# Performance work log

Hardware: AMD Instinct MI355X
Metric: run time of the kernel (lower is better)

Reference implementation:

```python
import jax, jax.numpy as jnp
import numpy as np

DIM = 64
NUM_HEADS = 8
HEAD_DIM = DIM // NUM_HEADS
INF = 1e9
EPS = 1e-10
S, R = 2048, 512  # n_seq (MSA rows), n_res


def setup_inputs() -> dict:
    key = jax.random.key(0)
    ks = jax.random.split(key, 8)
    m = jax.random.normal(ks[0], (S, R, DIM), dtype=jnp.float32)
    attn_mask = jnp.ones((S, R), dtype=jnp.float32)
    # weights stored as [in, out] (torch Linear applies x @ W.T; equivalent math)
    Wq = jax.random.normal(ks[1], (DIM, NUM_HEADS * HEAD_DIM), dtype=jnp.float32) * (DIM ** -0.5)
    Wk = jax.random.normal(ks[2], (DIM, HEAD_DIM), dtype=jnp.float32) * (DIM ** -0.5)
    Wv = jax.random.normal(ks[3], (DIM, HEAD_DIM), dtype=jnp.float32) * (DIM ** -0.5)
    Wg = jax.random.normal(ks[4], (DIM, NUM_HEADS * HEAD_DIM), dtype=jnp.float32) * (DIM ** -0.5)
    bg = jnp.ones((NUM_HEADS * HEAD_DIM,), dtype=jnp.float32)  # gating init: bias=1
    Wo = jax.random.normal(ks[5], (NUM_HEADS * HEAD_DIM, DIM), dtype=jnp.float32) * (DIM ** -0.5)
    bo = jnp.zeros((DIM,), dtype=jnp.float32)
    return {"m": m, "attn_mask": attn_mask, "Wq": Wq, "Wk": Wk, "Wv": Wv,
            "Wg": Wg, "bg": bg, "Wo": Wo, "bo": bo}


def reference(m, attn_mask, Wq, Wk, Wv, Wg, bg, Wo, bo):
    # masked mean-pool over residue axis -> per-row query  [S, dim]
    q = jnp.sum(m * attn_mask[..., None], axis=-2) / (jnp.sum(attn_mask, axis=-1)[..., None] + EPS)
    q = (q @ Wq).reshape(S, NUM_HEADS, HEAD_DIM) * (HEAD_DIM ** -0.5)  # [S, H, hd]
    k = m @ Wk  # [S, R, hd] (single shared K/V head)
    v = m @ Wv  # [S, R, hd]
    a = jnp.einsum('shc,src->shr', q, k)  # [S, H, R]
    a = a + (INF * (attn_mask - 1.0))[:, None, :]
    a = jax.nn.softmax(a, axis=-1)
    o = jnp.einsum('shr,src->shc', a, v)  # [S, H, hd]
    g = jax.nn.sigmoid(m @ Wg + bg).reshape(S, R, NUM_HEADS, HEAD_DIM)  # [S, R, H, hd]
    o = o[:, None, :, :] * g  # broadcast pooled output across residues
    o = o.reshape(S, R, NUM_HEADS * HEAD_DIM)
    return o @ Wo + bo  # [S, R, dim]
```

## Files before the change

kernel.cpp:

```cpp
#include <hip/hip_runtime.h>
#include <hip/hip_bf16.h>
#include <math.h>

#define NS 2048
#define NR 512
#define ND 64
#define NH 8
#define NSLOT 18

typedef __attribute__((ext_vector_type(4))) float f4;
typedef __attribute__((ext_vector_type(4))) unsigned u4;
typedef __attribute__((ext_vector_type(2))) unsigned u2;
typedef __attribute__((ext_vector_type(8))) short s8;

__device__ __forceinline__ short f2bf(float f) {
  unsigned u = __builtin_bit_cast(unsigned, f);
  u += 0x7fffu + ((u >> 16) & 1u);
  return (short)(u >> 16);
}
__device__ __forceinline__ unsigned cvtpk(float lo, float hi) {
  unsigned r;
  asm("v_cvt_pk_bf16_f32 %0, %1, %2" : "=v"(r) : "v"(lo), "v"(hi));
  return r;
}
__device__ __forceinline__ float bflo(unsigned u) { return __builtin_bit_cast(float, u << 16); }
__device__ __forceinline__ float bfhi(unsigned u) { return __builtin_bit_cast(float, u & 0xffff0000u); }

__device__ __forceinline__ int swz(int r, int c) {
  return ((r << 7) + (c << 1)) ^ ((r & 7) << 4);
}
__device__ __forceinline__ int kvaddr(int r, int c) {
  return ((r << 5) + (c << 1)) ^ ((r & 4) << 2);
}

__global__ void prep_kernel(const float* __restrict__ Wk, const float* __restrict__ Wv,
                            const float* __restrict__ Wg, const float* __restrict__ Wo,
                            short* __restrict__ ws) {
  for (int i = threadIdx.x; i < NSLOT * 64; i += blockDim.x) {
    const int slot = i >> 6, lane = i & 63;
    const int col = lane & 15, kq = (lane >> 4) * 8;
    s8 f;
    if (slot < 2) {
      #pragma unroll
      for (int jj = 0; jj < 8; ++jj) {
        const int k = slot * 32 + kq + jj;
        f[jj] = f2bf(col < 8 ? Wk[k * 8 + col] : Wv[k * 8 + col - 8]);
      }
    } else if (slot < 10) {
      const int idx = slot - 2, ks = idx >> 2, nt = idx & 3;
      #pragma unroll
      for (int jj = 0; jj < 8; ++jj) {
        const int k = ks * 32 + kq + jj;
        f[jj] = f2bf(Wg[k * 64 + 4 * col + nt]);
      }
    } else {
      const int idx = slot - 10, ks = idx >> 2, nt = idx & 3;
      #pragma unroll
      for (int jj = 0; jj < 8; ++jj) {
        const int k = ks * 32 + kq + jj;
        f[jj] = f2bf(Wo[k * 64 + 4 * col + nt]);
      }
    }
    *reinterpret_cast<s8*>(ws + (size_t)i * 8) = f;
  }
}

__global__ __launch_bounds__(512, 6)
void ga_kernel(const float* __restrict__ gm, const float* __restrict__ gmask,
               const float* __restrict__ Wq, const float* __restrict__ bgp,
               const float* __restrict__ bop, const short* __restrict__ ws,
               float* __restrict__ gout)
{
  __shared__ short fragB[NSLOT * 64 * 8];
  __shared__ union {
    unsigned short kv[NR][16];
    short tmp[8][16 * ND];
  } ukv;
  __shared__ float maskb[NR];
  __shared__ float red[8][ND];
  __shared__ float ofl[ND];
  __shared__ float bgo[2][ND];

  const int t    = threadIdx.x;
  const int lane = t & 63;
  const int wv   = t >> 6;
  const int s    = blockIdx.x;

  const int arow = lane & 15;
  const int g    = lane >> 4;
  const int kq   = g * 8;

  const float* mrow = gm + (size_t)s * NR * ND;

  for (int i = t; i < NR; i += 512) maskb[i] = gmask[(size_t)s * NR + i];
  for (int i = t; i < NSLOT * 64; i += 512)
    *reinterpret_cast<s8*>(&fragB[i * 8]) =
        *reinterpret_cast<const s8*>(ws + (size_t)i * 8);
  if (t < 64)            bgo[0][t]      = bgp[t];
  else if (t < 128)      bgo[1][t - 64] = bop[t - 64];
  __syncthreads();

  f4 pA0 = {0,0,0,0}, pA1 = {0,0,0,0}, pB0 = {0,0,0,0}, pB1 = {0,0,0,0};
  #pragma unroll
  for (int mt = 0; mt < 4; ++mt) {
    const int row = wv * 64 + mt * 16 + arow;
    const float mk = maskb[row];
    const float* p = mrow + row * ND + kq;
    const f4 a0 = *reinterpret_cast<const f4*>(p);
    const f4 a1 = *reinterpret_cast<const f4*>(p + 4);
    const f4 b0 = *reinterpret_cast<const f4*>(p + 32);
    const f4 b1 = *reinterpret_cast<const f4*>(p + 36);
    pA0 += a0 * mk; pA1 += a1 * mk; pB0 += b0 * mk; pB1 += b1 * mk;
    u4 ua, ub;
    ua[0] = cvtpk(a0.x, a0.y); ua[1] = cvtpk(a0.z, a0.w);
    ua[2] = cvtpk(a1.x, a1.y); ua[3] = cvtpk(a1.z, a1.w);
    ub[0] = cvtpk(b0.x, b0.y); ub[1] = cvtpk(b0.z, b0.w);
    ub[2] = cvtpk(b1.x, b1.y); ub[3] = cvtpk(b1.z, b1.w);
    const s8 mA = __builtin_bit_cast(s8, ua);
    const s8 mB = __builtin_bit_cast(s8, ub);
    const s8 kf0 = *reinterpret_cast<const s8*>(&fragB[(0 * 64 + lane) * 8]);
    const s8 kf1 = *reinterpret_cast<const s8*>(&fragB[(1 * 64 + lane) * 8]);
    f4 acc = {0,0,0,0};
    acc = __builtin_amdgcn_mfma_f32_16x16x32_bf16(mA, kf0, acc, 0, 0, 0);
    acc = __builtin_amdgcn_mfma_f32_16x16x32_bf16(mB, kf1, acc, 0, 0, 0);
    const int r0 = wv * 64 + mt * 16;
    #pragma unroll
    for (int q = 0; q < 4; ++q)
      *reinterpret_cast<unsigned short*>(
          reinterpret_cast<char*>(ukv.kv) + kvaddr(r0 + g * 4 + q, arow)) =
          (unsigned short)f2bf(acc[q]);
  }
  #pragma unroll
  for (int off = 8; off >= 1; off >>= 1) {
    pA0.x += __shfl_xor(pA0.x, off); pA0.y += __shfl_xor(pA0.y, off);
    pA0.z += __shfl_xor(pA0.z, off); pA0.w += __shfl_xor(pA0.w, off);
    pA1.x += __shfl_xor(pA1.x, off); pA1.y += __shfl_xor(pA1.y, off);
    pA1.z += __shfl_xor(pA1.z, off); pA1.w += __shfl_xor(pA1.w, off);
    pB0.x += __shfl_xor(pB0.x, off); pB0.y += __shfl_xor(pB0.y, off);
    pB0.z += __shfl_xor(pB0.z, off); pB0.w += __shfl_xor(pB0.w, off);
    pB1.x += __shfl_xor(pB1.x, off); pB1.y += __shfl_xor(pB1.y, off);
    pB1.z += __shfl_xor(pB1.z, off); pB1.w += __shfl_xor(pB1.w, off);
  }
  if (arow == 0) {
    *reinterpret_cast<f4*>(&red[wv][kq])          = pA0;
    *reinterpret_cast<f4*>(&red[wv][kq + 4])      = pA1;
    *reinterpret_cast<f4*>(&red[wv][32 + kq])     = pB0;
    *reinterpret_cast<f4*>(&red[wv][32 + kq + 4]) = pB1;
  }
  __syncthreads();

  f4 pf0, pf1, pf2, pf3;
  {
    const float* p = mrow + (wv * 64 + arow) * ND + kq;
    pf0 = *reinterpret_cast<const f4*>(p);
    pf1 = *reinterpret_cast<const f4*>(p + 4);
    pf2 = *reinterpret_cast<const f4*>(p + 32);
    pf3 = *reinterpret_cast<const f4*>(p + 36);
  }

  float q0, q1, q2, q3, q4, q5, q6, q7;
  {
    float qv_l = 0.f;
    #pragma unroll
    for (int p = 0; p < 8; ++p) qv_l += red[p][lane];
    float dn = 0.f;
    #pragma unroll
    for (int i = 0; i < 8; ++i) dn += maskb[lane + 64 * i];
    #pragma unroll
    for (int off = 32; off; off >>= 1) dn += __shfl_xor(dn, off);
    const f4 w0 = *reinterpret_cast<const f4*>(Wq + lane * 64 + wv * 8);
    const f4 w1 = *reinterpret_cast<const f4*>(Wq + lane * 64 + wv * 8 + 4);
    float a0 = qv_l * w0.x, a1 = qv_l * w0.y, a2 = qv_l * w0.z, a3 = qv_l * w0.w;
    float a4 = qv_l * w1.x, a5 = qv_l * w1.y, a6 = qv_l * w1.z, a7 = qv_l * w1.w;
    #pragma unroll
    for (int off = 32; off; off >>= 1) {
      a0 += __shfl_xor(a0, off); a1 += __shfl_xor(a1, off);
      a2 += __shfl_xor(a2, off); a3 += __shfl_xor(a3, off);
      a4 += __shfl_xor(a4, off); a5 += __shfl_xor(a5, off);
      a6 += __shfl_xor(a6, off); a7 += __shfl_xor(a7, off);
    }
    const float qs = 0.35355339059327373f / (dn + 1e-10f);
    q0 = a0 * qs; q1 = a1 * qs; q2 = a2 * qs; q3 = a3 * qs;
    q4 = a4 * qs; q5 = a5 * qs; q6 = a6 * qs; q7 = a7 * qs;
  }

  {
    float lg[8];
    float mx = -3.4e38f;
    #pragma unroll
    for (int i = 0; i < 8; ++i) {
      const int r = lane + 64 * i;
      const u4 kk = *reinterpret_cast<const u4*>(
          reinterpret_cast<const char*>(ukv.kv) + ((r << 5) ^ ((r & 4) << 2)));
      float acc = q0 * bflo(kk[0]) + q1 * bfhi(kk[0])
                + q2 * bflo(kk[1]) + q3 * bfhi(kk[1])
                + q4 * bflo(kk[2]) + q5 * bfhi(kk[2])
                + q6 * bflo(kk[3]) + q7 * bfhi(kk[3]);
      lg[i] = acc + 1e9f * (maskb[r] - 1.0f);
      mx = fmaxf(mx, lg[i]);
    }
    #pragma unroll
    for (int off = 32; off; off >>= 1) mx = fmaxf(mx, __shfl_xor(mx, off));
    float sum = 0.f;
    #pragma unroll
    for (int i = 0; i < 8; ++i) { lg[i] = __expf(lg[i] - mx); sum += lg[i]; }
    #pragma unroll
    for (int off = 32; off; off >>= 1) sum += __shfl_xor(sum, off);
    const float inv = 1.0f / sum;
    float po[8] = {0,0,0,0,0,0,0,0};
    #pragma unroll
    for (int i = 0; i < 8; ++i) {
      const int r = lane + 64 * i;
      const float a = lg[i] * inv;
      const u4 vvv = *reinterpret_cast<const u4*>(
          reinterpret_cast<const char*>(ukv.kv) + (((r << 5) + 16) ^ ((r & 4) << 2)));
      po[0] += a * bflo(vvv[0]); po[1] += a * bfhi(vvv[0]);
      po[2] += a * bflo(vvv[1]); po[3] += a * bfhi(vvv[1]);
      po[4] += a * bflo(vvv[2]); po[5] += a * bfhi(vvv[2]);
      po[6] += a * bflo(vvv[3]); po[7] += a * bfhi(vvv[3]);
    }
    #pragma unroll
    for (int off = 32; off; off >>= 1) {
      #pragma unroll
      for (int c = 0; c < 8; ++c) po[c] += __shfl_xor(po[c], off);
    }
    #pragma unroll
    for (int c = 0; c < 8; ++c) if (lane == c) ofl[wv * 8 + c] = po[c];
  }
  __syncthreads();

  short* tmpw = &ukv.tmp[wv][0];
  float* orow_base = gout + (size_t)s * NR * ND;
  const f4 zf = {0,0,0,0};

  #pragma unroll
  for (int mt = 0; mt < 4; ++mt) {
    const int r0 = wv * 64 + mt * 16;
    f4 a0, a1, b0, b1;
    if (mt == 0) { a0 = pf0; a1 = pf1; b0 = pf2; b1 = pf3; }
    else {
      const float* p = mrow + (r0 + arow) * ND + kq;
      a0 = *reinterpret_cast<const f4*>(p);
      a1 = *reinterpret_cast<const f4*>(p + 4);
      b0 = *reinterpret_cast<const f4*>(p + 32);
      b1 = *reinterpret_cast<const f4*>(p + 36);
    }
    u4 ua, ub;
    ua[0] = cvtpk(a0.x, a0.y); ua[1] = cvtpk(a0.z, a0.w);
    ua[2] = cvtpk(a1.x, a1.y); ua[3] = cvtpk(a1.z, a1.w);
    ub[0] = cvtpk(b0.x, b0.y); ub[1] = cvtpk(b0.z, b0.w);
    ub[2] = cvtpk(b1.x, b1.y); ub[3] = cvtpk(b1.z, b1.w);
    const s8 mA = __builtin_bit_cast(s8, ua);
    const s8 mB = __builtin_bit_cast(s8, ub);

    f4 accG[4] = {zf, zf, zf, zf};
    #pragma unroll
    for (int nt = 0; nt < 4; ++nt) {
      const s8 wg0 = *reinterpret_cast<const s8*>(&fragB[((2 + nt) * 64 + lane) * 8]);
      const s8 wg1 = *reinterpret_cast<const s8*>(&fragB[((6 + nt) * 64 + lane) * 8]);
      accG[nt] = __builtin_amdgcn_mfma_f32_16x16x32_bf16(mA, wg0, accG[nt], 0, 0, 0);
      accG[nt] = __builtin_amdgcn_mfma_f32_16x16x32_bf16(mB, wg1, accG[nt], 0, 0, 0);
    }

    const f4 ofv = *reinterpret_cast<const f4*>(&ofl[4 * arow]);
    const f4 bgv = *reinterpret_cast<const f4*>(&bgo[0][4 * arow]);
    #pragma unroll
    for (int q = 0; q < 4; ++q) {
      float v[4];
      #pragma unroll
      for (int nt = 0; nt < 4; ++nt)
        v[nt] = ofv[nt] / (1.0f + __expf(-(accG[nt][q] + bgv[nt])));
      u2 w;
      w[0] = cvtpk(v[0], v[1]);
      w[1] = cvtpk(v[2], v[3]);
      *reinterpret_cast<u2*>(reinterpret_cast<char*>(tmpw) + swz(g * 4 + q, 4 * arow)) = w;
    }
    asm volatile("s_waitcnt lgkmcnt(0)" ::: "memory");
    __builtin_amdgcn_sched_barrier(0);

    f4 accO[4] = {zf, zf, zf, zf};
    #pragma unroll
    for (int ks = 0; ks < 2; ++ks) {
      const s8 aF = *reinterpret_cast<const s8*>(
          reinterpret_cast<const char*>(tmpw) + swz(arow, ks * 32 + kq));
      #pragma unroll
      for (int nt = 0; nt < 4; ++nt) {
        const s8 woF = *reinterpret_cast<const s8*>(&fragB[((10 + ks * 4 + nt) * 64 + lane) * 8]);
        accO[nt] = __builtin_amdgcn_mfma_f32_16x16x32_bf16(aF, woF, accO[nt], 0, 0, 0);
      }
    }
    const f4 bov = *reinterpret_cast<const f4*>(&bgo[1][4 * arow]);
    #pragma unroll
    for (int q = 0; q < 4; ++q) {
      f4 ov;
      ov.x = accO[0][q] + bov.x;
      ov.y = accO[1][q] + bov.y;
      ov.z = accO[2][q] + bov.z;
      ov.w = accO[3][q] + bov.w;
      *reinterpret_cast<f4*>(orow_base + (r0 + g * 4 + q) * ND + 4 * arow) = ov;
    }
  }
}

extern "C" void kernel_launch(void* const* d_in, const int* in_sizes, int n_in,
                              void* d_out, int out_size, void* d_ws, size_t ws_size,
                              hipStream_t stream) {
  const float* m    = (const float*)d_in[0];
  const float* mask = (const float*)d_in[1];
  const float* Wq   = (const float*)d_in[2];
  const float* Wk   = (const float*)d_in[3];
  const float* Wv   = (const float*)d_in[4];
  const float* Wg   = (const float*)d_in[5];
  const float* bg   = (const float*)d_in[6];
  const float* Wo   = (const float*)d_in[7];
  const float* bo   = (const float*)d_in[8];
  float* out = (float*)d_out;
  short* ws  = (short*)d_ws;

  prep_kernel<<<dim3(1), dim3(512), 0, stream>>>(Wk, Wv, Wg, Wo, ws);
  ga_kernel<<<dim3(NS), dim3(512), 0, stream>>>(m, mask, Wq, bg, bo, ws, out);
}
```

Measured before the change: 152.8 us.

## Halve block size to 256 threads and read weight fragments from global

Each block now uses 4 waves instead of 8. Each wave handles 128 rows and two heads of the attention, and the occupancy hint rises to 8 blocks. The shared-memory copy of the bf16 weight fragments is removed, and the fragments are loaded straight from the workspace in global memory, where they should stay in cache. This shrinks LDS use and per-block sync cost, but each wave does more sequential work. It also trades LDS reads for global/L2 reads inside the inner MFMA loops, and the prefetch of the first m tile is dropped.

```diff
diff --git a/kernel.cpp b/kernel.cpp
--- a/kernel.cpp
+++ b/kernel.cpp
@@ -65,19 +65,18 @@
   }
 }
 
-__global__ __launch_bounds__(512, 6)
+__global__ __launch_bounds__(256, 8)
 void ga_kernel(const float* __restrict__ gm, const float* __restrict__ gmask,
                const float* __restrict__ Wq, const float* __restrict__ bgp,
                const float* __restrict__ bop, const short* __restrict__ ws,
                float* __restrict__ gout)
 {
-  __shared__ short fragB[NSLOT * 64 * 8];
   __shared__ union {
     unsigned short kv[NR][16];
-    short tmp[8][16 * ND];
+    short tmp[4][16 * ND];
   } ukv;
   __shared__ float maskb[NR];
-  __shared__ float red[8][ND];
+  __shared__ float red[4][ND];
   __shared__ float ofl[ND];
   __shared__ float bgo[2][ND];
 
@@ -92,18 +91,17 @@
 
   const float* mrow = gm + (size_t)s * NR * ND;
 
-  for (int i = t; i < NR; i += 512) maskb[i] = gmask[(size_t)s * NR + i];
-  for (int i = t; i < NSLOT * 64; i += 512)
-    *reinterpret_cast<s8*>(&fragB[i * 8]) =
-        *reinterpret_cast<const s8*>(ws + (size_t)i * 8);
+  for (int i = t; i < NR; i += 256) maskb[i] = gmask[(size_t)s * NR + i];
   if (t < 64)            bgo[0][t]      = bgp[t];
   else if (t < 128)      bgo[1][t - 64] = bop[t - 64];
+  const s8 kf0 = *reinterpret_cast<const s8*>(ws + (size_t)(0 * 64 + lane) * 8);
+  const s8 kf1 = *reinterpret_cast<const s8*>(ws + (size_t)(1 * 64 + lane) * 8);
   __syncthreads();
 
   f4 pA0 = {0,0,0,0}, pA1 = {0,0,0,0}, pB0 = {0,0,0,0}, pB1 = {0,0,0,0};
   #pragma unroll
-  for (int mt = 0; mt < 4; ++mt) {
-    const int row = wv * 64 + mt * 16 + arow;
+  for (int mt = 0; mt < 8; ++mt) {
+    const int row = wv * 128 + mt * 16 + arow;
     const float mk = maskb[row];
     const float* p = mrow + row * ND + kq;
     const f4 a0 = *reinterpret_cast<const f4*>(p);
@@ -118,12 +116,10 @@
     ub[2] = cvtpk(b1.x, b1.y); ub[3] = cvtpk(b1.z, b1.w);
     const s8 mA = __builtin_bit_cast(s8, ua);
     const s8 mB = __builtin_bit_cast(s8, ub);
-    const s8 kf0 = *reinterpret_cast<const s8*>(&fragB[(0 * 64 + lane) * 8]);
-    const s8 kf1 = *reinterpret_cast<const s8*>(&fragB[(1 * 64 + lane) * 8]);
     f4 acc = {0,0,0,0};
     acc = __builtin_amdgcn_mfma_f32_16x16x32_bf16(mA, kf0, acc, 0, 0, 0);
     acc = __builtin_amdgcn_mfma_f32_16x16x32_bf16(mB, kf1, acc, 0, 0, 0);
-    const int r0 = wv * 64 + mt * 16;
+    const int r0 = wv * 128 + mt * 16;
     #pragma unroll
     for (int q = 0; q < 4; ++q)
       *reinterpret_cast<unsigned short*>(
@@ -149,42 +145,36 @@
   }
   __syncthreads();
 
-  f4 pf0, pf1, pf2, pf3;
+  float qv_l, qs;
   {
-    const float* p = mrow + (wv * 64 + arow) * ND + kq;
-    pf0 = *reinterpret_cast<const f4*>(p);
-    pf1 = *reinterpret_cast<const f4*>(p + 4);
-    pf2 = *reinterpret_cast<const f4*>(p + 32);
-    pf3 = *reinterpret_cast<const f4*>(p + 36);
-  }
-
-  float q0, q1, q2, q3, q4, q5, q6, q7;
-  {
-    float qv_l = 0.f;
-    #pragma unroll
-    for (int p = 0; p < 8; ++p) qv_l += red[p][lane];
+    qv_l = red[0][lane] + red[1][lane] + red[2][lane] + red[3][lane];
     float dn = 0.f;
     #pragma unroll
     for (int i = 0; i < 8; ++i) dn += maskb[lane + 64 * i];
     #pragma unroll
     for (int off = 32; off; off >>= 1) dn += __shfl_xor(dn, off);
-    const f4 w0 = *reinterpret_cast<const f4*>(Wq + lane * 64 + wv * 8);
-    const f4 w1 = *reinterpret_cast<const f4*>(Wq + lane * 64 + wv * 8 + 4);
-    float a0 = qv_l * w0.x, a1 = qv_l * w0.y, a2 = qv_l * w0.z, a3 = qv_l * w0.w;
-    float a4 = qv_l * w1.x, a5 = qv_l * w1.y, a6 = qv_l * w1.z, a7 = qv_l * w1.w;
-    #pragma unroll
-    for (int off = 32; off; off >>= 1) {
-      a0 += __shfl_xor(a0, off); a1 += __shfl_xor(a1, off);
-      a2 += __shfl_xor(a2, off); a3 += __shfl_xor(a3, off);
-      a4 += __shfl_xor(a4, off); a5 += __shfl_xor(a5, off);
-      a6 += __shfl_xor(a6, off); a7 += __shfl_xor(a7, off);
-    }
-    const float qs = 0.35355339059327373f / (dn + 1e-10f);
-    q0 = a0 * qs; q1 = a1 * qs; q2 = a2 * qs; q3 = a3 * qs;
-    q4 = a4 * qs; q5 = a5 * qs; q6 = a6 * qs; q7 = a7 * qs;
-  }
-
-  {
+    qs = 0.35355339059327373f / (dn + 1e-10f);
+  }
+
+  #pragma unroll
+  for (int h2 = 0; h2 < 2; ++h2) {
+    const int h = wv * 2 + h2;
+    float q0, q1, q2, q3, q4, q5, q6, q7;
+    {
+      const f4 w0 = *reinterpret_cast<const f4*>(Wq + lane * 64 + h * 8);
+      const f4 w1 = *reinterpret_cast<const f4*>(Wq + lane * 64 + h * 8 + 4);
+      float a0 = qv_l * w0.x, a1 = qv_l * w0.y, a2 = qv_l * w0.z, a3 = qv_l * w0.w;
+      float a4 = qv_l * w1.x, a5 = qv_l * w1.y, a6 = qv_l * w1.z, a7 = qv_l * w1.w;
+      #pragma unroll
+      for (int off = 32; off; off >>= 1) {
+        a0 += __shfl_xor(a0, off); a1 += __shfl_xor(a1, off);
+        a2 += __shfl_xor(a2, off); a3 += __shfl_xor(a3, off);
+        a4 += __shfl_xor(a4, off); a5 += __shfl_xor(a5, off);
+        a6 += __shfl_xor(a6, off); a7 += __shfl_xor(a7, off);
+      }
+      q0 = a0 * qs; q1 = a1 * qs; q2 = a2 * qs; q3 = a3 * qs;
+      q4 = a4 * qs; q5 = a5 * qs; q6 = a6 * qs; q7 = a7 * qs;
+    }
     float lg[8];
     float mx = -3.4e38f;
     #pragma unroll
@@ -225,26 +215,25 @@
       for (int c = 0; c < 8; ++c) po[c] += __shfl_xor(po[c], off);
     }
     #pragma unroll
-    for (int c = 0; c < 8; ++c) if (lane == c) ofl[wv * 8 + c] = po[c];
+    for (int c = 0; c < 8; ++c) if (lane == c) ofl[h * 8 + c] = po[c];
   }
   __syncthreads();
 
   short* tmpw = &ukv.tmp[wv][0];
   float* orow_base = gout + (size_t)s * NR * ND;
   const f4 zf = {0,0,0,0};
+  const f4 ofv = *reinterpret_cast<const f4*>(&ofl[4 * arow]);
+  const f4 bgv = *reinterpret_cast<const f4*>(&bgo[0][4 * arow]);
+  const f4 bov = *reinterpret_cast<const f4*>(&bgo[1][4 * arow]);
 
   #pragma unroll
-  for (int mt = 0; mt < 4; ++mt) {
-    const int r0 = wv * 64 + mt * 16;
-    f4 a0, a1, b0, b1;
-    if (mt == 0) { a0 = pf0; a1 = pf1; b0 = pf2; b1 = pf3; }
-    else {
-      const float* p = mrow + (r0 + arow) * ND + kq;
-      a0 = *reinterpret_cast<const f4*>(p);
-      a1 = *reinterpret_cast<const f4*>(p + 4);
-      b0 = *reinterpret_cast<const f4*>(p + 32);
-      b1 = *reinterpret_cast<const f4*>(p + 36);
-    }
+  for (int mt = 0; mt < 8; ++mt) {
+    const int r0 = wv * 128 + mt * 16;
+    const float* p = mrow + (r0 + arow) * ND + kq;
+    const f4 a0 = *reinterpret_cast<const f4*>(p);
+    const f4 a1 = *reinterpret_cast<const f4*>(p + 4);
+    const f4 b0 = *reinterpret_cast<const f4*>(p + 32);
+    const f4 b1 = *reinterpret_cast<const f4*>(p + 36);
     u4 ua, ub;
     ua[0] = cvtpk(a0.x, a0.y); ua[1] = cvtpk(a0.z, a0.w);
     ua[2] = cvtpk(a1.x, a1.y); ua[3] = cvtpk(a1.z, a1.w);
@@ -256,14 +245,12 @@
     f4 accG[4] = {zf, zf, zf, zf};
     #pragma unroll
     for (int nt = 0; nt < 4; ++nt) {
-      const s8 wg0 = *reinterpret_cast<const s8*>(&fragB[((2 + nt) * 64 + lane) * 8]);
-      const s8 wg1 = *reinterpret_cast<const s8*>(&fragB[((6 + nt) * 64 + lane) * 8]);
+      const s8 wg0 = *reinterpret_cast<const s8*>(ws + (size_t)((2 + nt) * 64 + lane) * 8);
+      const s8 wg1 = *reinterpret_cast<const s8*>(ws + (size_t)((6 + nt) * 64 + lane) * 8);
       accG[nt] = __builtin_amdgcn_mfma_f32_16x16x32_bf16(mA, wg0, accG[nt], 0, 0, 0);
       accG[nt] = __builtin_amdgcn_mfma_f32_16x16x32_bf16(mB, wg1, accG[nt], 0, 0, 0);
     }
 
-    const f4 ofv = *reinterpret_cast<const f4*>(&ofl[4 * arow]);
-    const f4 bgv = *reinterpret_cast<const f4*>(&bgo[0][4 * arow]);
     #pragma unroll
     for (int q = 0; q < 4; ++q) {
       float v[4];
@@ -285,11 +272,10 @@
           reinterpret_cast<const char*>(tmpw) + swz(arow, ks * 32 + kq));
       #pragma unroll
       for (int nt = 0; nt < 4; ++nt) {
-        const s8 woF = *reinterpret_cast<const s8*>(&fragB[((10 + ks * 4 + nt) * 64 + lane) * 8]);
+        const s8 woF = *reinterpret_cast<const s8*>(ws + (size_t)((10 + ks * 4 + nt) * 64 + lane) * 8);
         accO[nt] = __builtin_amdgcn_mfma_f32_16x16x32_bf16(aF, woF, accO[nt], 0, 0, 0);
       }
     }
-    const f4 bov = *reinterpret_cast<const f4*>(&bgo[1][4 * arow]);
     #pragma unroll
     for (int q = 0; q < 4; ++q) {
       f4 ov;
@@ -317,6 +303,6 @@
   float* out = (float*)d_out;
   short* ws  = (short*)d_ws;
 
-  prep_kernel<<<dim3(1), dim3(512), 0, stream>>>(Wk, Wv, Wg, Wo, ws);
-  ga_kernel<<<dim3(NS), dim3(512), 0, stream>>>(m, mask, Wq, bg, bo, ws, out);
-}
+  prep_kernel<<<dim3(1), dim3(256), 0, stream>>>(Wk, Wv, Wg, Wo, ws);
+  ga_kernel<<<dim3(NS), dim3(256), 0, stream>>>(m, mask, Wq, bg, bo, ws, out);
+}
```

Result: slower. 255.0 us (+66.9%).

## Process four MSA rows per block and overlap next row's pooling with gating

Applied to the files above, without the earlier changes.

Each block now handles four sequence rows and software-pipelines them. The K/V projection and masked pooling for row j+1 are interleaved with the gating and output projection of row j, so that global load latency is hidden behind MFMA work. Per-block setup of the weight fragments is also amortised over four rows. The cost is fewer blocks (512 instead of 2048), lower occupancy (launch bounds 6 to 4), and more LDS, since the K/V and temp buffers are no longer unioned.

```diff
diff --git a/kernel.cpp b/kernel.cpp
--- a/kernel.cpp
+++ b/kernel.cpp
@@ -7,6 +7,7 @@
 #define ND 64
 #define NH 8
 #define NSLOT 18
+#define SPB 4
 
 typedef __attribute__((ext_vector_type(4))) float f4;
 typedef __attribute__((ext_vector_type(4))) unsigned u4;
@@ -65,18 +66,16 @@
   }
 }
 
-__global__ __launch_bounds__(512, 6)
+__global__ __launch_bounds__(512, 4)
 void ga_kernel(const float* __restrict__ gm, const float* __restrict__ gmask,
                const float* __restrict__ Wq, const float* __restrict__ bgp,
                const float* __restrict__ bop, const short* __restrict__ ws,
                float* __restrict__ gout)
 {
   __shared__ short fragB[NSLOT * 64 * 8];
-  __shared__ union {
-    unsigned short kv[NR][16];
-    short tmp[8][16 * ND];
-  } ukv;
-  __shared__ float maskb[NR];
+  __shared__ unsigned short kvb_s[NR * 16];
+  __shared__ short tmpb[8][16 * ND];
+  __shared__ float maskb[SPB][NR];
   __shared__ float red[8][ND];
   __shared__ float ofl[ND];
   __shared__ float bgo[2][ND];
@@ -84,33 +83,27 @@
   const int t    = threadIdx.x;
   const int lane = t & 63;
   const int wv   = t >> 6;
-  const int s    = blockIdx.x;
-
   const int arow = lane & 15;
   const int g    = lane >> 4;
   const int kq   = g * 8;
-
-  const float* mrow = gm + (size_t)s * NR * ND;
-
-  for (int i = t; i < NR; i += 512) maskb[i] = gmask[(size_t)s * NR + i];
+  const int s0   = blockIdx.x * SPB;
+
+  const f4 zf = {0, 0, 0, 0};
+
   for (int i = t; i < NSLOT * 64; i += 512)
-    *reinterpret_cast<s8*>(&fragB[i * 8]) =
-        *reinterpret_cast<const s8*>(ws + (size_t)i * 8);
-  if (t < 64)            bgo[0][t]      = bgp[t];
-  else if (t < 128)      bgo[1][t - 64] = bop[t - 64];
+    *reinterpret_cast<s8*>(&fragB[i * 8]) = *reinterpret_cast<const s8*>(ws + (size_t)i * 8);
+  for (int i = t; i < SPB * NR; i += 512)
+    (&maskb[0][0])[i] = gmask[(size_t)s0 * NR + i];
+  if (t < 64)       bgo[0][t]      = bgp[t];
+  else if (t < 128) bgo[1][t - 64] = bop[t - 64];
   __syncthreads();
 
-  f4 pA0 = {0,0,0,0}, pA1 = {0,0,0,0}, pB0 = {0,0,0,0}, pB1 = {0,0,0,0};
-  #pragma unroll
-  for (int mt = 0; mt < 4; ++mt) {
+  f4 pl0, pl1, pl2, pl3;
+
+  auto a_finish = [&](int mt, int jn, f4 a0, f4 a1, f4 b0, f4 b1) {
     const int row = wv * 64 + mt * 16 + arow;
-    const float mk = maskb[row];
-    const float* p = mrow + row * ND + kq;
-    const f4 a0 = *reinterpret_cast<const f4*>(p);
-    const f4 a1 = *reinterpret_cast<const f4*>(p + 4);
-    const f4 b0 = *reinterpret_cast<const f4*>(p + 32);
-    const f4 b1 = *reinterpret_cast<const f4*>(p + 36);
-    pA0 += a0 * mk; pA1 += a1 * mk; pB0 += b0 * mk; pB1 += b1 * mk;
+    const float mk = maskb[jn][row];
+    pl0 += a0 * mk; pl1 += a1 * mk; pl2 += b0 * mk; pl3 += b1 * mk;
     u4 ua, ub;
     ua[0] = cvtpk(a0.x, a0.y); ua[1] = cvtpk(a0.z, a0.w);
     ua[2] = cvtpk(a1.x, a1.y); ua[3] = cvtpk(a1.z, a1.w);
@@ -120,52 +113,44 @@
     const s8 mB = __builtin_bit_cast(s8, ub);
     const s8 kf0 = *reinterpret_cast<const s8*>(&fragB[(0 * 64 + lane) * 8]);
     const s8 kf1 = *reinterpret_cast<const s8*>(&fragB[(1 * 64 + lane) * 8]);
-    f4 acc = {0,0,0,0};
+    f4 acc = zf;
     acc = __builtin_amdgcn_mfma_f32_16x16x32_bf16(mA, kf0, acc, 0, 0, 0);
     acc = __builtin_amdgcn_mfma_f32_16x16x32_bf16(mB, kf1, acc, 0, 0, 0);
+    char* kvb = reinterpret_cast<char*>(&kvb_s[0]);
     const int r0 = wv * 64 + mt * 16;
     #pragma unroll
     for (int q = 0; q < 4; ++q)
-      *reinterpret_cast<unsigned short*>(
-          reinterpret_cast<char*>(ukv.kv) + kvaddr(r0 + g * 4 + q, arow)) =
+      *reinterpret_cast<unsigned short*>(kvb + kvaddr(r0 + g * 4 + q, arow)) =
           (unsigned short)f2bf(acc[q]);
-  }
-  #pragma unroll
-  for (int off = 8; off >= 1; off >>= 1) {
-    pA0.x += __shfl_xor(pA0.x, off); pA0.y += __shfl_xor(pA0.y, off);
-    pA0.z += __shfl_xor(pA0.z, off); pA0.w += __shfl_xor(pA0.w, off);
-    pA1.x += __shfl_xor(pA1.x, off); pA1.y += __shfl_xor(pA1.y, off);
-    pA1.z += __shfl_xor(pA1.z, off); pA1.w += __shfl_xor(pA1.w, off);
-    pB0.x += __shfl_xor(pB0.x, off); pB0.y += __shfl_xor(pB0.y, off);
-    pB0.z += __shfl_xor(pB0.z, off); pB0.w += __shfl_xor(pB0.w, off);
-    pB1.x += __shfl_xor(pB1.x, off); pB1.y += __shfl_xor(pB1.y, off);
-    pB1.z += __shfl_xor(pB1.z, off); pB1.w += __shfl_xor(pB1.w, off);
-  }
-  if (arow == 0) {
-    *reinterpret_cast<f4*>(&red[wv][kq])          = pA0;
-    *reinterpret_cast<f4*>(&red[wv][kq + 4])      = pA1;
-    *reinterpret_cast<f4*>(&red[wv][32 + kq])     = pB0;
-    *reinterpret_cast<f4*>(&red[wv][32 + kq + 4]) = pB1;
-  }
-  __syncthreads();
-
-  f4 pf0, pf1, pf2, pf3;
-  {
-    const float* p = mrow + (wv * 64 + arow) * ND + kq;
-    pf0 = *reinterpret_cast<const f4*>(p);
-    pf1 = *reinterpret_cast<const f4*>(p + 4);
-    pf2 = *reinterpret_cast<const f4*>(p + 32);
-    pf3 = *reinterpret_cast<const f4*>(p + 36);
-  }
-
-  float q0, q1, q2, q3, q4, q5, q6, q7;
-  {
+  };
+
+  auto a_end = [&]() {
+    #pragma unroll
+    for (int off = 8; off >= 1; off >>= 1) {
+      pl0.x += __shfl_xor(pl0.x, off); pl0.y += __shfl_xor(pl0.y, off);
+      pl0.z += __shfl_xor(pl0.z, off); pl0.w += __shfl_xor(pl0.w, off);
+      pl1.x += __shfl_xor(pl1.x, off); pl1.y += __shfl_xor(pl1.y, off);
+      pl1.z += __shfl_xor(pl1.z, off); pl1.w += __shfl_xor(pl1.w, off);
+      pl2.x += __shfl_xor(pl2.x, off); pl2.y += __shfl_xor(pl2.y, off);
+      pl2.z += __shfl_xor(pl2.z, off); pl2.w += __shfl_xor(pl2.w, off);
+      pl3.x += __shfl_xor(pl3.x, off); pl3.y += __shfl_xor(pl3.y, off);
+      pl3.z += __shfl_xor(pl3.z, off); pl3.w += __shfl_xor(pl3.w, off);
+    }
+    if (arow == 0) {
+      *reinterpret_cast<f4*>(&red[wv][kq])          = pl0;
+      *reinterpret_cast<f4*>(&red[wv][kq + 4])      = pl1;
+      *reinterpret_cast<f4*>(&red[wv][32 + kq])     = pl2;
+      *reinterpret_cast<f4*>(&red[wv][32 + kq + 4]) = pl3;
+    }
+  };
+
+  auto attn = [&](int j) {
     float qv_l = 0.f;
     #pragma unroll
-    for (int p = 0; p < 8; ++p) qv_l += red[p][lane];
+    for (int w = 0; w < 8; ++w) qv_l += red[w][lane];
     float dn = 0.f;
     #pragma unroll
-    for (int i = 0; i < 8; ++i) dn += maskb[lane + 64 * i];
+    for (int i = 0; i < 8; ++i) dn += maskb[j][lane + 64 * i];
     #pragma unroll
     for (int off = 32; off; off >>= 1) dn += __shfl_xor(dn, off);
     const f4 w0 = *reinterpret_cast<const f4*>(Wq + lane * 64 + wv * 8);
@@ -180,23 +165,21 @@
       a6 += __shfl_xor(a6, off); a7 += __shfl_xor(a7, off);
     }
     const float qs = 0.35355339059327373f / (dn + 1e-10f);
-    q0 = a0 * qs; q1 = a1 * qs; q2 = a2 * qs; q3 = a3 * qs;
-    q4 = a4 * qs; q5 = a5 * qs; q6 = a6 * qs; q7 = a7 * qs;
-  }
-
-  {
+    const float q0 = a0 * qs, q1 = a1 * qs, q2 = a2 * qs, q3 = a3 * qs;
+    const float q4 = a4 * qs, q5 = a5 * qs, q6 = a6 * qs, q7 = a7 * qs;
+
+    const char* kvb = reinterpret_cast<const char*>(&kvb_s[0]);
     float lg[8];
     float mx = -3.4e38f;
     #pragma unroll
     for (int i = 0; i < 8; ++i) {
       const int r = lane + 64 * i;
-      const u4 kk = *reinterpret_cast<const u4*>(
-          reinterpret_cast<const char*>(ukv.kv) + ((r << 5) ^ ((r & 4) << 2)));
+      const u4 kk = *reinterpret_cast<const u4*>(kvb + ((r << 5) ^ ((r & 4) << 2)));
       float acc = q0 * bflo(kk[0]) + q1 * bfhi(kk[0])
                 + q2 * bflo(kk[1]) + q3 * bfhi(kk[1])
                 + q4 * bflo(kk[2]) + q5 * bfhi(kk[2])
                 + q6 * bflo(kk[3]) + q7 * bfhi(kk[3]);
-      lg[i] = acc + 1e9f * (maskb[r] - 1.0f);
+      lg[i] = acc + 1e9f * (maskb[j][r] - 1.0f);
       mx = fmaxf(mx, lg[i]);
     }
     #pragma unroll
@@ -207,13 +190,12 @@
     #pragma unroll
     for (int off = 32; off; off >>= 1) sum += __shfl_xor(sum, off);
     const float inv = 1.0f / sum;
-    float po[8] = {0,0,0,0,0,0,0,0};
+    float po[8] = {0, 0, 0, 0, 0, 0, 0, 0};
     #pragma unroll
     for (int i = 0; i < 8; ++i) {
       const int r = lane + 64 * i;
       const float a = lg[i] * inv;
-      const u4 vvv = *reinterpret_cast<const u4*>(
-          reinterpret_cast<const char*>(ukv.kv) + (((r << 5) + 16) ^ ((r & 4) << 2)));
+      const u4 vvv = *reinterpret_cast<const u4*>(kvb + (((r << 5) + 16) ^ ((r & 4) << 2)));
       po[0] += a * bflo(vvv[0]); po[1] += a * bfhi(vvv[0]);
       po[2] += a * bflo(vvv[1]); po[3] += a * bfhi(vvv[1]);
       po[4] += a * bflo(vvv[2]); po[5] += a * bfhi(vvv[2]);
@@ -226,25 +208,15 @@
     }
     #pragma unroll
     for (int c = 0; c < 8; ++c) if (lane == c) ofl[wv * 8 + c] = po[c];
-  }
-  __syncthreads();
-
-  short* tmpw = &ukv.tmp[wv][0];
-  float* orow_base = gout + (size_t)s * NR * ND;
-  const f4 zf = {0,0,0,0};
-
-  #pragma unroll
-  for (int mt = 0; mt < 4; ++mt) {
+  };
+
+  auto b_iter = [&](int mt, const float* mrowB, float* orow) {
     const int r0 = wv * 64 + mt * 16;
-    f4 a0, a1, b0, b1;
-    if (mt == 0) { a0 = pf0; a1 = pf1; b0 = pf2; b1 = pf3; }
-    else {
-      const float* p = mrow + (r0 + arow) * ND + kq;
-      a0 = *reinterpret_cast<const f4*>(p);
-      a1 = *reinterpret_cast<const f4*>(p + 4);
-      b0 = *reinterpret_cast<const f4*>(p + 32);
-      b1 = *reinterpret_cast<const f4*>(p + 36);
-    }
+    const float* p = mrowB + (r0 + arow) * ND + kq;
+    const f4 a0 = *reinterpret_cast<const f4*>(p);
+    const f4 a1 = *reinterpret_cast<const f4*>(p + 4);
+    const f4 b0 = *reinterpret_cast<const f4*>(p + 32);
+    const f4 b1 = *reinterpret_cast<const f4*>(p + 36);
     u4 ua, ub;
     ua[0] = cvtpk(a0.x, a0.y); ua[1] = cvtpk(a0.z, a0.w);
     ua[2] = cvtpk(a1.x, a1.y); ua[3] = cvtpk(a1.z, a1.w);
@@ -264,16 +236,17 @@
 
     const f4 ofv = *reinterpret_cast<const f4*>(&ofl[4 * arow]);
     const f4 bgv = *reinterpret_cast<const f4*>(&bgo[0][4 * arow]);
-    #pragma unroll
-    for (int q = 0; q < 4; ++q) {
+    short* tmpw = &tmpb[wv][0];
+    #pragma unroll
+    for (int q2 = 0; q2 < 4; ++q2) {
       float v[4];
       #pragma unroll
       for (int nt = 0; nt < 4; ++nt)
-        v[nt] = ofv[nt] / (1.0f + __expf(-(accG[nt][q] + bgv[nt])));
+        v[nt] = ofv[nt] / (1.0f + __expf(-(accG[nt][q2] + bgv[nt])));
       u2 w;
       w[0] = cvtpk(v[0], v[1]);
       w[1] = cvtpk(v[2], v[3]);
-      *reinterpret_cast<u2*>(reinterpret_cast<char*>(tmpw) + swz(g * 4 + q, 4 * arow)) = w;
+      *reinterpret_cast<u2*>(reinterpret_cast<char*>(tmpw) + swz(g * 4 + q2, 4 * arow)) = w;
     }
     asm volatile("s_waitcnt lgkmcnt(0)" ::: "memory");
     __builtin_amdgcn_sched_barrier(0);
@@ -291,14 +264,59 @@
     }
     const f4 bov = *reinterpret_cast<const f4*>(&bgo[1][4 * arow]);
     #pragma unroll
-    for (int q = 0; q < 4; ++q) {
+    for (int q2 = 0; q2 < 4; ++q2) {
       f4 ov;
-      ov.x = accO[0][q] + bov.x;
-      ov.y = accO[1][q] + bov.y;
-      ov.z = accO[2][q] + bov.z;
-      ov.w = accO[3][q] + bov.w;
-      *reinterpret_cast<f4*>(orow_base + (r0 + g * 4 + q) * ND + 4 * arow) = ov;
-    }
+      ov.x = accO[0][q2] + bov.x;
+      ov.y = accO[1][q2] + bov.y;
+      ov.z = accO[2][q2] + bov.z;
+      ov.w = accO[3][q2] + bov.w;
+      *reinterpret_cast<f4*>(orow + (r0 + g * 4 + q2) * ND + 4 * arow) = ov;
+    }
+  };
+
+  pl0 = pl1 = pl2 = pl3 = zf;
+  {
+    const float* mA_ = gm + (size_t)s0 * NR * ND;
+    #pragma unroll 1
+    for (int mt = 0; mt < 4; ++mt) {
+      const float* p = mA_ + (wv * 64 + mt * 16 + arow) * ND + kq;
+      const f4 a0 = *reinterpret_cast<const f4*>(p);
+      const f4 a1 = *reinterpret_cast<const f4*>(p + 4);
+      const f4 b0 = *reinterpret_cast<const f4*>(p + 32);
+      const f4 b1 = *reinterpret_cast<const f4*>(p + 36);
+      a_finish(mt, 0, a0, a1, b0, b1);
+    }
+    a_end();
+  }
+  __syncthreads();
+
+  #pragma unroll 1
+  for (int j = 0; j < SPB; ++j) {
+    attn(j);
+    __syncthreads();
+
+    const float* mB_ = gm + (size_t)(s0 + j) * NR * ND;
+    float* oB_ = gout + (size_t)(s0 + j) * NR * ND;
+
+    if (j < SPB - 1) {
+      pl0 = pl1 = pl2 = pl3 = zf;
+      const float* mA_ = gm + (size_t)(s0 + j + 1) * NR * ND;
+      #pragma unroll 1
+      for (int mt = 0; mt < 4; ++mt) {
+        const float* pa = mA_ + (wv * 64 + mt * 16 + arow) * ND + kq;
+        const f4 a0 = *reinterpret_cast<const f4*>(pa);
+        const f4 a1 = *reinterpret_cast<const f4*>(pa + 4);
+        const f4 b0 = *reinterpret_cast<const f4*>(pa + 32);
+        const f4 b1 = *reinterpret_cast<const f4*>(pa + 36);
+        b_iter(mt, mB_, oB_);
+        a_finish(mt, j + 1, a0, a1, b0, b1);
+      }
+      a_end();
+    } else {
+      #pragma unroll 1
+      for (int mt = 0; mt < 4; ++mt) b_iter(mt, mB_, oB_);
+    }
+    __syncthreads();
   }
 }
 
@@ -318,5 +336,5 @@
   short* ws  = (short*)d_ws;
 
   prep_kernel<<<dim3(1), dim3(512), 0, stream>>>(Wk, Wv, Wg, Wo, ws);
-  ga_kernel<<<dim3(NS), dim3(512), 0, stream>>>(m, mask, Wq, bg, bo, ws, out);
-}
+  ga_kernel<<<dim3(NS / SPB), dim3(512), 0, stream>>>(m, mask, Wq, bg, bo, ws, out);
+}
```

Measured after the change: 164.8 us. 7.9% more time.
